# Performance work log

Measured on AMD Instinct MI355X. Metric: run time of the kernel, lower is better.

## Reference

```python
import jax, jax.numpy as jnp
import numpy as np

N_NODES = 100000
N_EDGES = 1600000
N_GRAPHS = 1024
DIM_IN = 128
DIM_SF = 32
DIM_OUT = 8
EPS = 1e-5


def setup_inputs() -> dict:
    key = jax.random.key(0)
    ks = jax.random.split(key, 16)
    feat = jax.random.normal(ks[0], (N_NODES, DIM_IN), dtype=jnp.float32)
    self_feat = jax.random.normal(ks[1], (N_GRAPHS, DIM_SF), dtype=jnp.float32)
    src = jax.random.randint(ks[2], (N_EDGES,), 0, N_NODES)
    dst = jax.random.randint(ks[3], (N_EDGES,), 0, N_NODES)
    node2graph = jnp.sort(jax.random.randint(ks[4], (N_NODES,), 0, N_GRAPHS))

    def lin(k, din, dout):
        s = 1.0 / np.sqrt(din)
        kw, kb = jax.random.split(k)
        W = jax.random.uniform(kw, (din, dout), minval=-s, maxval=s, dtype=jnp.float32)
        b = jax.random.uniform(kb, (dout,), minval=-s, maxval=s, dtype=jnp.float32)
        return W, b

    W1, b1 = lin(ks[5], DIM_IN, 100)
    W2, b2 = lin(ks[6], 100, 20)
    Wf1, bf1 = lin(ks[7], 20 * DIM_SF, 128)
    Wf2, bf2 = lin(ks[8], 128, 32)
    Wf3, bf3 = lin(ks[9], 32, DIM_OUT)
    g1 = jnp.ones((128,), jnp.float32); be1 = jnp.zeros((128,), jnp.float32)
    g2 = jnp.ones((32,), jnp.float32); be2 = jnp.zeros((32,), jnp.float32)
    return dict(feat=feat, self_feat=self_feat, src=src, dst=dst,
                node2graph=node2graph, W1=W1, b1=b1, W2=W2, b2=b2,
                Wf1=Wf1, bf1=bf1, g1=g1, be1=be1,
                Wf2=Wf2, bf2=bf2, g2=g2, be2=be2, Wf3=Wf3, bf3=bf3)


def _gcn_layer(h, src, dst, W, b):
    # copy_u + mean reduce: segment-mean of source features onto destinations.
    n = h.shape[0]
    msum = jax.ops.segment_sum(h[src], dst, num_segments=n)        # [N, d]
    deg = jax.ops.segment_sum(jnp.ones((src.shape[0], 1), h.dtype), dst,
                              num_segments=n)                      # [N, 1]
    # DGL: nodes with no incoming messages keep their previous 'h'.
    agg = jnp.where(deg > 0, msum / jnp.maximum(deg, 1.0), h)
    return agg @ W + b


def _bn(x, gamma, beta):
    # BatchNorm1d in training mode: biased batch statistics.
    mu = jnp.mean(x, axis=0)
    var = jnp.mean((x - mu) ** 2, axis=0)
    return (x - mu) / jnp.sqrt(var + EPS) * gamma + beta


def reference(feat, self_feat, src, dst, node2graph,
              W1, b1, W2, b2, Wf1, bf1, g1, be1, Wf2, bf2, g2, be2, Wf3, bf3):
    h = jax.nn.relu(_gcn_layer(feat, src, dst, W1, b1))            # [N, 100]
    h = jax.nn.relu(_gcn_layer(h, src, dst, W2, b2))               # [N, 20]
    # dgl.mean_nodes: per-graph mean pooling
    hsum = jax.ops.segment_sum(h, node2graph, num_segments=N_GRAPHS)
    cnt = jax.ops.segment_sum(jnp.ones((h.shape[0], 1), h.dtype), node2graph,
                              num_segments=N_GRAPHS)
    hg = hsum / jnp.maximum(cnt, 1.0)                              # [G, 20]
    # Kronecker fusion: bmm(hg[:, :, None], self_feat[:, None, :])
    fused = (hg[:, :, None] * self_feat[:, None, :]).reshape(hg.shape[0], -1)
    out = jax.nn.relu(_bn(fused @ Wf1 + bf1, g1, be1))
    out = jax.nn.relu(_bn(out @ Wf2 + bf2, g2, be2))
    return out @ Wf3 + bf3                                         # [G, 8]
```

## Files before the change

### kernel.cpp

```cpp
#include <hip/hip_runtime.h>
#include <hip/hip_fp16.h>

#define N_NODES 100000
#define N_EDGES 1600000
#define N_GRAPHS 1024
#define DIM_IN 128
#define D1 100
#define D1P 128
#define D2 20
#define D2P 32
#define DIM_SF 32
#define DF1 128
#define DF2 32
#define DOUT 8
#define EPS 1e-5f

typedef _Float16 hh2 __attribute__((ext_vector_type(2)));

__device__ __forceinline__ void fdacc(unsigned u, float& lo, float& hi) {
  const hh2 MLO = {(_Float16)1.0f, (_Float16)0.0f};
  const hh2 MHI = {(_Float16)0.0f, (_Float16)1.0f};
  hh2 h = __builtin_bit_cast(hh2, u);
  lo = __builtin_amdgcn_fdot2(h, MLO, lo, false);
  hi = __builtin_amdgcn_fdot2(h, MHI, hi, false);
}

__device__ __forceinline__ unsigned pkadd(unsigned a, unsigned b) {
  __half2 x = __builtin_bit_cast(__half2, a);
  __half2 y = __builtin_bit_cast(__half2, b);
  return __builtin_bit_cast(unsigned, __hadd2(x, y));
}

#define NBK 512
#define BW 196
#define EPB 4096
#define NBLK1 ((N_EDGES + EPB - 1) / EPB)

__global__ void __launch_bounds__(256) k_bcount(const int* __restrict__ dst,
                                                int* __restrict__ counts) {
  __shared__ int hist[NBK];
  int t = threadIdx.x, blk = blockIdx.x;
  for (int i = t; i < NBK; i += 256) hist[i] = 0;
  __syncthreads();
  int base = blk * EPB;
#pragma unroll
  for (int r = 0; r < 16; r++) {
    int e = base + r * 256 + t;
    if (e < N_EDGES) {
      unsigned b = (unsigned)dst[e] / BW;
      atomicAdd(&hist[b], 1);
    }
  }
  __syncthreads();
  for (int i = t; i < NBK; i += 256) counts[blk * NBK + i] = hist[i];
}

__global__ void __launch_bounds__(64) k_bscanA(const int* __restrict__ counts,
                                               int* __restrict__ offs,
                                               int* __restrict__ totals) {
  int b = blockIdx.x, l = threadIdx.x;
  int carry = 0;
  for (int chunk = 0; chunk < NBLK1; chunk += 64) {
    int blk = chunk + l;
    int v = (blk < NBLK1) ? counts[blk * NBK + b] : 0;
    int incl = v;
    for (int s = 1; s < 64; s <<= 1) { int x = __shfl_up(incl, s); if (l >= s) incl += x; }
    if (blk < NBLK1) offs[blk * NBK + b] = carry + incl - v;
    carry += __shfl(incl, 63);
  }
  if (l == 0) totals[b] = carry;
}

__global__ void __launch_bounds__(512) k_bscanB(const int* __restrict__ totals,
                                                int* __restrict__ bin_base) {
  __shared__ int lds[NBK];
  int t = threadIdx.x;
  int v = totals[t];
  lds[t] = v; __syncthreads();
  for (int s = 1; s < NBK; s <<= 1) {
    int x = (t >= s) ? lds[t - s] : 0;
    __syncthreads();
    lds[t] += x;
    __syncthreads();
  }
  bin_base[t] = lds[t] - v;
  if (t == NBK - 1) bin_base[NBK] = lds[t];
}

__global__ void __launch_bounds__(256) k_bscatter(const int* __restrict__ src,
                                                  const int* __restrict__ dst,
                                                  const int* __restrict__ offs,
                                                  const int* __restrict__ bin_base,
                                                  unsigned* __restrict__ packed_out) {
  __shared__ int hist[NBK];
  __shared__ int lbase[NBK];
  __shared__ int gbase[NBK];
  __shared__ int ssum[256];
  __shared__ unsigned sval[EPB];
  __shared__ int spos[EPB];
  int t = threadIdx.x, blk = blockIdx.x;
  for (int i = t; i < NBK; i += 256) hist[i] = 0;
  __syncthreads();
  int base = blk * EPB;
  unsigned pk[16]; int bn[16]; int rk[16];
#pragma unroll
  for (int r = 0; r < 16; r++) {
    int e = base + r * 256 + t;
    bn[r] = -1;
    if (e < N_EDGES) {
      int dv = dst[e];
      unsigned b = (unsigned)dv / BW;
      unsigned ld = (unsigned)dv - b * BW;
      bn[r] = (int)b;
      pk[r] = ((unsigned)src[e] << 8) | ld;
      rk[r] = atomicAdd(&hist[b], 1);
    }
  }
  __syncthreads();
  int h0 = hist[2 * t], h1 = hist[2 * t + 1];
  int s = h0 + h1;
  ssum[t] = s; __syncthreads();
  for (int off = 1; off < 256; off <<= 1) {
    int x = (t >= off) ? ssum[t - off] : 0;
    __syncthreads();
    ssum[t] += x;
    __syncthreads();
  }
  int excl = ssum[t] - s;
  lbase[2 * t] = excl;
  lbase[2 * t + 1] = excl + h0;
  gbase[2 * t]     = bin_base[2 * t]     + offs[blk * NBK + 2 * t];
  gbase[2 * t + 1] = bin_base[2 * t + 1] + offs[blk * NBK + 2 * t + 1];
  __syncthreads();
#pragma unroll
  for (int r = 0; r < 16; r++) {
    if (bn[r] >= 0) {
      int li = lbase[bn[r]] + rk[r];
      sval[li] = pk[r];
      spos[li] = gbase[bn[r]] + rk[r];
    }
  }
  __syncthreads();
  int cnt = N_EDGES - base; if (cnt > EPB) cnt = EPB;
  for (int i = t; i < cnt; i += 256) packed_out[spos[i]] = sval[i];
}

__global__ void __launch_bounds__(256) k_bfine(const unsigned* __restrict__ packed_in,
                                               const int* __restrict__ bin_base,
                                               int* __restrict__ csr,
                                               int* __restrict__ deg,
                                               int* __restrict__ row_off) {
  __shared__ unsigned sval[EPB];
  __shared__ int scsr[EPB];
  __shared__ int hist[256];
  __shared__ int soff[256];
  __shared__ int cur[256];
  int b = blockIdx.x, t = threadIdx.x;
  int start = bin_base[b];
  int cnt = bin_base[b + 1] - start;
  if (cnt > EPB) cnt = EPB;
  hist[t] = 0;
  __syncthreads();
  for (int i = t; i < cnt; i += 256) {
    unsigned v = packed_in[start + i];
    sval[i] = v;
    atomicAdd(&hist[v & 255u], 1);
  }
  __syncthreads();
  int h = hist[t];
  soff[t] = h; __syncthreads();
  for (int off = 1; off < 256; off <<= 1) {
    int x = (t >= off) ? soff[t - off] : 0;
    __syncthreads();
    soff[t] += x;
    __syncthreads();
  }
  int excl = soff[t] - h;
  cur[t] = excl;
  int n = b * BW + t;
  if (t < BW && n < N_NODES) { deg[n] = h; row_off[n] = start + excl; }
  __syncthreads();
  for (int i = t; i < cnt; i += 256) {
    unsigned v = sval[i];
    int pos = atomicAdd(&cur[v & 255u], 1);
    scsr[pos] = (int)(v >> 8);
  }
  __syncthreads();
  for (int i = t; i < cnt; i += 256) csr[start + i] = scsr[i];
}

__global__ void __launch_bounds__(256) k_goff(const int* __restrict__ n2g,
                                              int* __restrict__ g_off) {
  int g = blockIdx.x * 256 + threadIdx.x;
  if (g > N_GRAPHS) return;
  if (g == N_GRAPHS) { g_off[g] = N_NODES; return; }
  int lo = 0, hi = N_NODES;
  while (lo < hi) {
    int mid = (lo + hi) >> 1;
    if (n2g[mid] < g) lo = mid + 1; else hi = mid;
  }
  g_off[g] = lo;
}

__global__ void __launch_bounds__(256) k_gemm1(const float* __restrict__ feat,
                                               const float* __restrict__ W1,
                                               __half* __restrict__ p1h) {
  __shared__ float w1s[DIM_IN * D1];
  int t = threadIdx.x;
  for (int i = t; i < DIM_IN * D1; i += 256) w1s[i] = W1[i];
  __syncthreads();
  if (t >= 250) return;
  int q = t % 25, ng = t / 25;
  int n0 = blockIdx.x * 40 + ng * 4;
  int c0 = q * 4;
  float acc[4][4] = {{0.f}};
  const float* f0 = feat + (size_t)n0 * DIM_IN;
  for (int k = 0; k < DIM_IN; k += 4) {
    float4 w0 = *(const float4*)&w1s[(k + 0) * D1 + c0];
    float4 w1 = *(const float4*)&w1s[(k + 1) * D1 + c0];
    float4 w2 = *(const float4*)&w1s[(k + 2) * D1 + c0];
    float4 w3 = *(const float4*)&w1s[(k + 3) * D1 + c0];
#pragma unroll
    for (int j = 0; j < 4; j++) {
      float4 f = *(const float4*)(f0 + j * DIM_IN + k);
      acc[j][0] += f.x * w0.x + f.y * w1.x + f.z * w2.x + f.w * w3.x;
      acc[j][1] += f.x * w0.y + f.y * w1.y + f.z * w2.y + f.w * w3.y;
      acc[j][2] += f.x * w0.z + f.y * w1.z + f.z * w2.z + f.w * w3.z;
      acc[j][3] += f.x * w0.w + f.y * w1.w + f.z * w2.w + f.w * w3.w;
    }
  }
#pragma unroll
  for (int j = 0; j < 4; j++) {
    __half2* d2 = (__half2*)(p1h + (size_t)(n0 + j) * D1P + c0);
    d2[0] = __floats2half2_rn(acc[j][0], acc[j][1]);
    d2[1] = __floats2half2_rn(acc[j][2], acc[j][3]);
  }
}

__device__ __forceinline__ void acc8d(uint4 r, float4& A, float4& B) {
  fdacc(r.x, A.x, A.y);
  fdacc(r.y, A.z, A.w);
  fdacc(r.z, B.x, B.y);
  fdacc(r.w, B.z, B.w);
}

__global__ void __launch_bounds__(256) k_agg1(const __half* __restrict__ p1h,
                                              const int* __restrict__ deg,
                                              const int* __restrict__ row_off,
                                              const int* __restrict__ csr,
                                              const float* __restrict__ b1,
                                              const float* __restrict__ W2,
                                              __half* __restrict__ p2h) {
  __shared__ float w2s[D1 * D2];
  __shared__ float b1s[D1];
  __shared__ float hbuf[4][104];
  int t = threadIdx.x;
  for (int i = t; i < D1 * D2; i += 256) w2s[i] = W2[i];
  if (t < D1) b1s[t] = b1[t];
  __syncthreads();
  int w = t >> 6, lane = t & 63;
  int n = blockIdx.x * 4 + w;
  int g = lane >> 4, o = lane & 15;
  int d = deg[n], ro = row_off[n];
  float4 A = {0.f, 0.f, 0.f, 0.f}, B = {0.f, 0.f, 0.f, 0.f};
  const size_t oh = (size_t)(o * 8);
  if (d > 0) {
    for (int base = 0; base < d; base += 64) {
      int m = d - base; if (m > 64) m = 64;
      int sv = (lane < m) ? csr[ro + base + lane] : 0;
      int nr = m >> 2;
      int r = 0;
      for (; r + 1 < nr; r += 2) {
        int sA = __shfl(sv, r * 4 + g);
        int sB = __shfl(sv, r * 4 + 4 + g);
        uint4 ra = *(const uint4*)(p1h + (size_t)sA * D1P + oh);
        uint4 rb = *(const uint4*)(p1h + (size_t)sB * D1P + oh);
        uint4 rc;
        rc.x = pkadd(ra.x, rb.x); rc.y = pkadd(ra.y, rb.y);
        rc.z = pkadd(ra.z, rb.z); rc.w = pkadd(ra.w, rb.w);
        acc8d(rc, A, B);
      }
      if (r < nr) {
        int sA = __shfl(sv, r * 4 + g);
        uint4 ra = *(const uint4*)(p1h + (size_t)sA * D1P + oh);
        acc8d(ra, A, B);
      }
      int rem = m & 3;
      int sT = __shfl(sv, nr * 4 + g);
      if (rem && g < rem) {
        uint4 ra = *(const uint4*)(p1h + (size_t)sT * D1P + oh);
        acc8d(ra, A, B);
      }
    }
  } else {
    if (g == 0) {
      uint4 ra = *(const uint4*)(p1h + (size_t)n * D1P + oh);
      acc8d(ra, A, B);
    }
  }
  float v[8] = {A.x, A.y, A.z, A.w, B.x, B.y, B.z, B.w};
#pragma unroll
  for (int j = 0; j < 8; j++) {
    v[j] += __shfl_down(v[j], 32);
    v[j] += __shfl_down(v[j], 16);
  }
  if (lane < 13) {
    float inv = (d > 0) ? 1.0f / (float)d : 1.0f;
#pragma unroll
    for (int j = 0; j < 8; j++) {
      int ch = 8 * lane + j;
      if (ch < D1) hbuf[w][ch] = fmaxf(v[j] * inv + b1s[ch], 0.f);
    }
  }
  __syncthreads();
  int p = lane / 20;
  int j20 = lane - p * 20;
  int cbeg = (p == 0) ? 0 : (p == 1) ? 33 : 66;
  int cend = (p == 0) ? 33 : (p == 1) ? 66 : 100;
  if (p >= 3) { cbeg = 0; cend = 0; }
  float acc = 0.f;
  for (int c = cbeg; c < cend; c++) acc += hbuf[w][c] * w2s[c * D2 + j20];
  float t1 = __shfl_down(acc, 20);
  float t2 = __shfl_down(acc, 40);
  acc += t1 + t2;
  if (lane < D2)       p2h[(size_t)n * D2P + lane] = __float2half_rn(acc);
  else if (lane < D2P) p2h[(size_t)n * D2P + lane] = __float2half_rn(0.f);
}

__global__ void __launch_bounds__(512) k_agg2(const __half* __restrict__ p2h,
                                              const int* __restrict__ deg,
                                              const int* __restrict__ row_off,
                                              const int* __restrict__ csr,
                                              const float* __restrict__ b2,
                                              const int* __restrict__ g_off,
                                              float* __restrict__ hg) {
  __shared__ float ssum[D2];
  __shared__ float b2s[D2];
  int g = blockIdx.x, t = threadIdx.x;
  if (t < D2) { ssum[t] = 0.f; b2s[t] = b2[t]; }
  __syncthreads();
  const unsigned* pu = (const unsigned*)p2h;
  int n_lo = g_off[g], n_hi = g_off[g + 1];
  int total = (n_hi - n_lo) * 10;
  for (int idx = t; idx < total; idx += 512) {
    int n = n_lo + idx / 10;
    int c2 = idx % 10;
    int d = deg[n], ro = row_off[n];
    float lo, hi;
    if (d > 0) {
      float l0 = 0.f, h0 = 0.f, l1 = 0.f, h1 = 0.f;
      int e = 0;
      for (; e + 3 < d; e += 4) {
        unsigned u0 = pu[(size_t)csr[ro + e]     * 16 + c2];
        unsigned u1 = pu[(size_t)csr[ro + e + 1] * 16 + c2];
        unsigned u2 = pu[(size_t)csr[ro + e + 2] * 16 + c2];
        unsigned u3 = pu[(size_t)csr[ro + e + 3] * 16 + c2];
        fdacc(u0, l0, h0); fdacc(u1, l1, h1);
        fdacc(u2, l0, h0); fdacc(u3, l1, h1);
      }
      for (; e < d; e++) {
        unsigned u = pu[(size_t)csr[ro + e] * 16 + c2];
        fdacc(u, l0, h0);
      }
      float inv = 1.0f / (float)d;
      lo = (l0 + l1) * inv; hi = (h0 + h1) * inv;
    } else {
      lo = 0.f; hi = 0.f;
      fdacc(pu[(size_t)n * 16 + c2], lo, hi);
    }
    atomicAdd(&ssum[2 * c2],     fmaxf(lo + b2s[2 * c2],     0.f));
    atomicAdd(&ssum[2 * c2 + 1], fmaxf(hi + b2s[2 * c2 + 1], 0.f));
  }
  __syncthreads();
  if (t < D2) {
    int cnt = n_hi - n_lo;
    float inv = (cnt > 0) ? 1.0f / (float)cnt : 0.f;
    hg[g * D2 + t] = ssum[t] * inv;
  }
}

__global__ void __launch_bounds__(128) k_mlp1(const float* __restrict__ hg,
                                              const float* __restrict__ sf,
                                              const float* __restrict__ Wf1,
                                              const float* __restrict__ bf1,
                                              float* __restrict__ y1) {
  __shared__ float prod[D2 * DIM_SF];
  __shared__ float hgl[D2], sfl[DIM_SF];
  int g = blockIdx.x, t = threadIdx.x;
  if (t < D2) hgl[t] = hg[g * D2 + t];
  if (t < DIM_SF) sfl[t] = sf[g * DIM_SF + t];
  __syncthreads();
  for (int i = t; i < D2 * DIM_SF; i += 128) prod[i] = hgl[i >> 5] * sfl[i & 31];
  __syncthreads();
  float acc = bf1[t];
#pragma unroll 4
  for (int k = 0; k < D2 * DIM_SF; k++) acc += prod[k] * Wf1[k * DF1 + t];
  y1[g * DF1 + t] = acc;
}

__global__ void k_bnstats(const float* __restrict__ x, int ld,
                          float* __restrict__ mu, float* __restrict__ rstd) {
  __shared__ float ssum[256], ssq[256];
  int c = blockIdx.x, t = threadIdx.x;
  float s = 0.f, q = 0.f;
  for (int r = t; r < N_GRAPHS; r += 256) { float v = x[r * ld + c]; s += v; q += v * v; }
  ssum[t] = s; ssq[t] = q; __syncthreads();
  for (int off = 128; off > 0; off >>= 1) {
    if (t < off) { ssum[t] += ssum[t + off]; ssq[t] += ssq[t + off]; }
    __syncthreads();
  }
  if (t == 0) {
    float m = ssum[0] / (float)N_GRAPHS;
    float var = ssq[0] / (float)N_GRAPHS - m * m;
    mu[c] = m;
    rstd[c] = rsqrtf(var + EPS);
  }
}

__global__ void k_mlp2(const float* __restrict__ y1, const float* __restrict__ mu1,
                       const float* __restrict__ rstd1, const float* __restrict__ g1,
                       const float* __restrict__ be1, const float* __restrict__ Wf2,
                       const float* __restrict__ bf2, float* __restrict__ y2) {
  int idx = blockIdx.x * 256 + threadIdx.x;
  int g = idx >> 5, o = idx & 31;
  float acc = bf2[o];
  for (int k = 0; k < DF1; k++) {
    float x = (y1[g * DF1 + k] - mu1[k]) * rstd1[k] * g1[k] + be1[k];
    x = fmaxf(x, 0.f);
    acc += x * Wf2[k * DF2 + o];
  }
  y2[g * DF2 + o] = acc;
}

__global__ void k_mlp3(const float* __restrict__ y2, const float* __restrict__ mu2,
                       const float* __restrict__ rstd2, const float* __restrict__ g2,
                       const float* __restrict__ be2, const float* __restrict__ Wf3,
                       const float* __restrict__ bf3, float* __restrict__ out) {
  int idx = blockIdx.x * 256 + threadIdx.x;
  int g = idx >> 3, o = idx & 7;
  float acc = bf3[o];
  for (int k = 0; k < DF2; k++) {
    float x = (y2[g * DF2 + k] - mu2[k]) * rstd2[k] * g2[k] + be2[k];
    x = fmaxf(x, 0.f);
    acc += x * Wf3[k * DOUT + o];
  }
  out[g * DOUT + o] = acc;
}

extern "C" void kernel_launch(void* const* d_in, const int* in_sizes, int n_in,
                              void* d_out, int out_size, void* d_ws, size_t ws_size,
                              hipStream_t stream) {
  const float* feat = (const float*)d_in[0];
  const float* sf   = (const float*)d_in[1];
  const int*   src  = (const int*)d_in[2];
  const int*   dst  = (const int*)d_in[3];
  const int*   n2g  = (const int*)d_in[4];
  const float* W1   = (const float*)d_in[5];
  const float* b1   = (const float*)d_in[6];
  const float* W2   = (const float*)d_in[7];
  const float* b2   = (const float*)d_in[8];
  const float* Wf1  = (const float*)d_in[9];
  const float* bf1  = (const float*)d_in[10];
  const float* g1   = (const float*)d_in[11];
  const float* be1  = (const float*)d_in[12];
  const float* Wf2  = (const float*)d_in[13];
  const float* bf2  = (const float*)d_in[14];
  const float* g2   = (const float*)d_in[15];
  const float* be2  = (const float*)d_in[16];
  const float* Wf3  = (const float*)d_in[17];
  const float* bf3  = (const float*)d_in[18];
  float* out = (float*)d_out;

  char* ws = (char*)d_ws;
  size_t off = 0;
  auto alloc = [&](size_t bytes) -> void* {
    void* p = ws + off;
    off = (off + bytes + 255) & ~(size_t)255;
    return p;
  };
  int*      g_offs   = (int*)alloc((N_GRAPHS + 1) * 4);
  float*    hg       = (float*)alloc(N_GRAPHS * D2 * 4);
  int*      deg      = (int*)alloc(N_NODES * 4);
  int*      row_off  = (int*)alloc(N_NODES * 4);
  int*      counts   = (int*)alloc((size_t)NBLK1 * NBK * 4);
  int*      offs     = (int*)alloc((size_t)NBLK1 * NBK * 4);
  int*      totals   = (int*)alloc(NBK * 4);
  int*      bin_base = (int*)alloc((NBK + 1) * 4);
  unsigned* packed   = (unsigned*)alloc((size_t)N_EDGES * 4);
  int*      csr      = (int*)alloc((size_t)N_EDGES * 4);
  __half*   p1h      = (__half*)alloc((size_t)N_NODES * D1P * 2);
  __half*   p2h      = (__half*)alloc((size_t)N_NODES * D2P * 2);
  float*    y1       = (float*)alloc((size_t)N_GRAPHS * DF1 * 4);
  float*    y2       = (float*)alloc((size_t)N_GRAPHS * DF2 * 4);
  float*    mu1      = (float*)alloc(DF1 * 4);
  float*    rstd1    = (float*)alloc(DF1 * 4);
  float*    mu2      = (float*)alloc(DF2 * 4);
  float*    rstd2    = (float*)alloc(DF2 * 4);

  k_goff<<<(N_GRAPHS + 1 + 255) / 256, 256, 0, stream>>>(n2g, g_offs);
  k_bcount<<<NBLK1, 256, 0, stream>>>(dst, counts);
  k_bscanA<<<NBK, 64, 0, stream>>>(counts, offs, totals);
  k_bscanB<<<1, NBK, 0, stream>>>(totals, bin_base);
  k_bscatter<<<NBLK1, 256, 0, stream>>>(src, dst, offs, bin_base, packed);
  k_bfine<<<NBK, 256, 0, stream>>>(packed, bin_base, csr, deg, row_off);
  k_gemm1<<<N_NODES / 40, 256, 0, stream>>>(feat, W1, p1h);
  k_agg1<<<N_NODES / 4, 256, 0, stream>>>(p1h, deg, row_off, csr, b1, W2, p2h);
  k_agg2<<<N_GRAPHS, 512, 0, stream>>>(p2h, deg, row_off, csr, b2, g_offs, hg);
  k_mlp1<<<N_GRAPHS, 128, 0, stream>>>(hg, sf, Wf1, bf1, y1);
  k_bnstats<<<DF1, 256, 0, stream>>>(y1, DF1, mu1, rstd1);
  k_mlp2<<<(N_GRAPHS * DF2) / 256, 256, 0, stream>>>(y1, mu1, rstd1, g1, be1, Wf2, bf2, y2);
  k_bnstats<<<DF2, 256, 0, stream>>>(y2, DF2, mu2, rstd2);
  k_mlp3<<<(N_GRAPHS * DOUT) / 256, 256, 0, stream>>>(y2, mu2, rstd2, g2, be2, Wf3, bf3, out);
}
```

Measured before the change: 400.9 us.

## Process several nodes per wave in agg1 and parallelize agg2 across edges

k_agg1 now has each wavefront handle 8 consecutive nodes in a loop. This spreads the per-block load of W2 and b1 into shared memory over more work and cuts the grid size. It also drops the block-wide barrier between writing and reading the per-wave hidden buffer, which relies on wavefront-local ordering. k_agg2 changes from one thread per (node, channel pair) walking edges serially to one wavefront per node: 8 edges are gathered in parallel with 8-byte loads, followed by a shuffle reduction and fewer shared atomics. The cost is that 3 of every 8 lanes sit idle in the gather, and load is uneven across waves when graph sizes vary.

```diff
diff --git a/kernel.cpp b/kernel.cpp
--- a/kernel.cpp
+++ b/kernel.cpp
@@ -14,6 +14,7 @@
 #define DF2 32
 #define DOUT 8
 #define EPS 1e-5f
+#define NPW 8
 
 typedef _Float16 hh2 __attribute__((ext_vector_type(2)));
 
@@ -259,72 +260,74 @@
   if (t < D1) b1s[t] = b1[t];
   __syncthreads();
   int w = t >> 6, lane = t & 63;
-  int n = blockIdx.x * 4 + w;
   int g = lane >> 4, o = lane & 15;
-  int d = deg[n], ro = row_off[n];
-  float4 A = {0.f, 0.f, 0.f, 0.f}, B = {0.f, 0.f, 0.f, 0.f};
   const size_t oh = (size_t)(o * 8);
-  if (d > 0) {
-    for (int base = 0; base < d; base += 64) {
-      int m = d - base; if (m > 64) m = 64;
-      int sv = (lane < m) ? csr[ro + base + lane] : 0;
-      int nr = m >> 2;
-      int r = 0;
-      for (; r + 1 < nr; r += 2) {
-        int sA = __shfl(sv, r * 4 + g);
-        int sB = __shfl(sv, r * 4 + 4 + g);
-        uint4 ra = *(const uint4*)(p1h + (size_t)sA * D1P + oh);
-        uint4 rb = *(const uint4*)(p1h + (size_t)sB * D1P + oh);
-        uint4 rc;
-        rc.x = pkadd(ra.x, rb.x); rc.y = pkadd(ra.y, rb.y);
-        rc.z = pkadd(ra.z, rb.z); rc.w = pkadd(ra.w, rb.w);
-        acc8d(rc, A, B);
-      }
-      if (r < nr) {
-        int sA = __shfl(sv, r * 4 + g);
-        uint4 ra = *(const uint4*)(p1h + (size_t)sA * D1P + oh);
-        acc8d(ra, A, B);
-      }
-      int rem = m & 3;
-      int sT = __shfl(sv, nr * 4 + g);
-      if (rem && g < rem) {
-        uint4 ra = *(const uint4*)(p1h + (size_t)sT * D1P + oh);
-        acc8d(ra, A, B);
-      }
-    }
-  } else {
-    if (g == 0) {
-      uint4 ra = *(const uint4*)(p1h + (size_t)n * D1P + oh);
-      acc8d(ra, A, B);
-    }
-  }
-  float v[8] = {A.x, A.y, A.z, A.w, B.x, B.y, B.z, B.w};
-#pragma unroll
-  for (int j = 0; j < 8; j++) {
-    v[j] += __shfl_down(v[j], 32);
-    v[j] += __shfl_down(v[j], 16);
-  }
-  if (lane < 13) {
-    float inv = (d > 0) ? 1.0f / (float)d : 1.0f;
-#pragma unroll
-    for (int j = 0; j < 8; j++) {
-      int ch = 8 * lane + j;
-      if (ch < D1) hbuf[w][ch] = fmaxf(v[j] * inv + b1s[ch], 0.f);
-    }
-  }
-  __syncthreads();
   int p = lane / 20;
   int j20 = lane - p * 20;
   int cbeg = (p == 0) ? 0 : (p == 1) ? 33 : 66;
   int cend = (p == 0) ? 33 : (p == 1) ? 66 : 100;
   if (p >= 3) { cbeg = 0; cend = 0; }
-  float acc = 0.f;
-  for (int c = cbeg; c < cend; c++) acc += hbuf[w][c] * w2s[c * D2 + j20];
-  float t1 = __shfl_down(acc, 20);
-  float t2 = __shfl_down(acc, 40);
-  acc += t1 + t2;
-  if (lane < D2)       p2h[(size_t)n * D2P + lane] = __float2half_rn(acc);
-  else if (lane < D2P) p2h[(size_t)n * D2P + lane] = __float2half_rn(0.f);
+  int n0 = (blockIdx.x * 4 + w) * NPW;
+  for (int nn = 0; nn < NPW; nn++) {
+    int n = n0 + nn;
+    int d = deg[n], ro = row_off[n];
+    float4 A = {0.f, 0.f, 0.f, 0.f}, B = {0.f, 0.f, 0.f, 0.f};
+    if (d > 0) {
+      for (int base = 0; base < d; base += 64) {
+        int m = d - base; if (m > 64) m = 64;
+        int sv = (lane < m) ? csr[ro + base + lane] : 0;
+        int nr = m >> 2;
+        int r = 0;
+        for (; r + 1 < nr; r += 2) {
+          int sA = __shfl(sv, r * 4 + g);
+          int sB = __shfl(sv, r * 4 + 4 + g);
+          uint4 ra = *(const uint4*)(p1h + (size_t)sA * D1P + oh);
+          uint4 rb = *(const uint4*)(p1h + (size_t)sB * D1P + oh);
+          uint4 rc;
+          rc.x = pkadd(ra.x, rb.x); rc.y = pkadd(ra.y, rb.y);
+          rc.z = pkadd(ra.z, rb.z); rc.w = pkadd(ra.w, rb.w);
+          acc8d(rc, A, B);
+        }
+        if (r < nr) {
+          int sA = __shfl(sv, r * 4 + g);
+          uint4 ra = *(const uint4*)(p1h + (size_t)sA * D1P + oh);
+          acc8d(ra, A, B);
+        }
+        int rem = m & 3;
+        int sT = __shfl(sv, nr * 4 + g);
+        if (rem && g < rem) {
+          uint4 ra = *(const uint4*)(p1h + (size_t)sT * D1P + oh);
+          acc8d(ra, A, B);
+        }
+      }
+    } else {
+      if (g == 0) {
+        uint4 ra = *(const uint4*)(p1h + (size_t)n * D1P + oh);
+        acc8d(ra, A, B);
+      }
+    }
+    float v[8] = {A.x, A.y, A.z, A.w, B.x, B.y, B.z, B.w};
+#pragma unroll
+    for (int j = 0; j < 8; j++) {
+      v[j] += __shfl_down(v[j], 32);
+      v[j] += __shfl_down(v[j], 16);
+    }
+    if (lane < 13) {
+      float inv = (d > 0) ? 1.0f / (float)d : 1.0f;
+#pragma unroll
+      for (int j = 0; j < 8; j++) {
+        int ch = 8 * lane + j;
+        if (ch < D1) hbuf[w][ch] = fmaxf(v[j] * inv + b1s[ch], 0.f);
+      }
+    }
+    float acc = 0.f;
+    for (int c = cbeg; c < cend; c++) acc += hbuf[w][c] * w2s[c * D2 + j20];
+    float t1 = __shfl_down(acc, 20);
+    float t2 = __shfl_down(acc, 40);
+    acc += t1 + t2;
+    if (lane < D2)       p2h[(size_t)n * D2P + lane] = __float2half_rn(acc);
+    else if (lane < D2P) p2h[(size_t)n * D2P + lane] = __float2half_rn(0.f);
+  }
 }
 
 __global__ void __launch_bounds__(512) k_agg2(const __half* __restrict__ p2h,
@@ -336,40 +339,58 @@
                                               float* __restrict__ hg) {
   __shared__ float ssum[D2];
   __shared__ float b2s[D2];
-  int g = blockIdx.x, t = threadIdx.x;
+  int t = threadIdx.x, w = t >> 6, lane = t & 63;
+  int g = blockIdx.x;
   if (t < D2) { ssum[t] = 0.f; b2s[t] = b2[t]; }
   __syncthreads();
   const unsigned* pu = (const unsigned*)p2h;
   int n_lo = g_off[g], n_hi = g_off[g + 1];
-  int total = (n_hi - n_lo) * 10;
-  for (int idx = t; idx < total; idx += 512) {
-    int n = n_lo + idx / 10;
-    int c2 = idx % 10;
+  int e8 = lane >> 3, o = lane & 7;
+  bool act = (o < 5);
+  for (int n = n_lo + w; n < n_hi; n += 8) {
     int d = deg[n], ro = row_off[n];
-    float lo, hi;
+    float4 A = {0.f, 0.f, 0.f, 0.f};
     if (d > 0) {
-      float l0 = 0.f, h0 = 0.f, l1 = 0.f, h1 = 0.f;
-      int e = 0;
-      for (; e + 3 < d; e += 4) {
-        unsigned u0 = pu[(size_t)csr[ro + e]     * 16 + c2];
-        unsigned u1 = pu[(size_t)csr[ro + e + 1] * 16 + c2];
-        unsigned u2 = pu[(size_t)csr[ro + e + 2] * 16 + c2];
-        unsigned u3 = pu[(size_t)csr[ro + e + 3] * 16 + c2];
-        fdacc(u0, l0, h0); fdacc(u1, l1, h1);
-        fdacc(u2, l0, h0); fdacc(u3, l1, h1);
+      for (int base = 0; base < d; base += 64) {
+        int m = d - base; if (m > 64) m = 64;
+        int sv = (lane < m) ? csr[ro + base + lane] : 0;
+        int nr = m >> 3;
+        for (int r = 0; r < nr; r++) {
+          int s0 = __shfl(sv, r * 8 + e8);
+          if (act) {
+            uint2 ra = *(const uint2*)(pu + (size_t)s0 * 16 + o * 2);
+            fdacc(ra.x, A.x, A.y);
+            fdacc(ra.y, A.z, A.w);
+          }
+        }
+        int rem = m & 7;
+        int sT = __shfl(sv, nr * 8 + e8);
+        if (e8 < rem && act) {
+          uint2 ra = *(const uint2*)(pu + (size_t)sT * 16 + o * 2);
+          fdacc(ra.x, A.x, A.y);
+          fdacc(ra.y, A.z, A.w);
+        }
       }
-      for (; e < d; e++) {
-        unsigned u = pu[(size_t)csr[ro + e] * 16 + c2];
-        fdacc(u, l0, h0);
+    } else if (e8 == 0 && act) {
+      uint2 ra = *(const uint2*)(pu + (size_t)n * 16 + o * 2);
+      fdacc(ra.x, A.x, A.y);
+      fdacc(ra.y, A.z, A.w);
+    }
+    float v[4] = {A.x, A.y, A.z, A.w};
+#pragma unroll
+    for (int j = 0; j < 4; j++) {
+      v[j] += __shfl_down(v[j], 32);
+      v[j] += __shfl_down(v[j], 16);
+      v[j] += __shfl_down(v[j], 8);
+    }
+    if (lane < 5) {
+      float inv = (d > 0) ? 1.0f / (float)d : 1.0f;
+#pragma unroll
+      for (int j = 0; j < 4; j++) {
+        int ch = 4 * lane + j;
+        atomicAdd(&ssum[ch], fmaxf(v[j] * inv + b2s[ch], 0.f));
       }
-      float inv = 1.0f / (float)d;
-      lo = (l0 + l1) * inv; hi = (h0 + h1) * inv;
-    } else {
-      lo = 0.f; hi = 0.f;
-      fdacc(pu[(size_t)n * 16 + c2], lo, hi);
-    }
-    atomicAdd(&ssum[2 * c2],     fmaxf(lo + b2s[2 * c2],     0.f));
-    atomicAdd(&ssum[2 * c2 + 1], fmaxf(hi + b2s[2 * c2 + 1], 0.f));
+    }
   }
   __syncthreads();
   if (t < D2) {
@@ -504,7 +525,7 @@
   k_bscatter<<<NBLK1, 256, 0, stream>>>(src, dst, offs, bin_base, packed);
   k_bfine<<<NBK, 256, 0, stream>>>(packed, bin_base, csr, deg, row_off);
   k_gemm1<<<N_NODES / 40, 256, 0, stream>>>(feat, W1, p1h);
-  k_agg1<<<N_NODES / 4, 256, 0, stream>>>(p1h, deg, row_off, csr, b1, W2, p2h);
+  k_agg1<<<N_NODES / (4 * NPW), 256, 0, stream>>>(p1h, deg, row_off, csr, b1, W2, p2h);
   k_agg2<<<N_GRAPHS, 512, 0, stream>>>(p2h, deg, row_off, csr, b2, g_offs, hg);
   k_mlp1<<<N_GRAPHS, 128, 0, stream>>>(hg, sf, Wf1, bf1, y1);
   k_bnstats<<<DF1, 256, 0, stream>>>(y1, DF1, mu1, rstd1);
```

Measured after the change: 402.0 us. No clear change (+0.3%).
